# Optimization experiments

Measured on AMD Instinct MI355X. Metric: run time of the kernel, lower is better.

Reference implementation:

```python
import jax, jax.numpy as jnp
import numpy as np

HAD_G = 32  # hadamard_group_size == MX block size (scales are [out, in//32])

# FP4 E2M1 magnitude grid and decision midpoints (round-to-nearest)
_FP4_LEVELS = jnp.array([0.0, 0.5, 1.0, 1.5, 2.0, 3.0, 4.0, 6.0], dtype=jnp.float32)
_FP4_MIDS = jnp.array([0.25, 0.75, 1.25, 1.75, 2.5, 3.5, 5.0], dtype=jnp.float32)


def _hadamard(n: int) -> np.ndarray:
    H = np.array([[1.0]], dtype=np.float32)
    while H.shape[0] < n:
        H = np.block([[H, H], [H, -H]])
    return H * (n ** -0.5)


def mxfp4_quant_dequant(v):
    """MXFP4 quantize-dequantize along the last axis (block of 32).
    v: [..., 32]. Shared power-of-2 scale per block (E8M0, absmax-based),
    elements rounded to nearest FP4 (E2M1) value. Straight-through estimator.
    """
    amax = jnp.max(jnp.abs(v), axis=-1, keepdims=True)
    # scale = 2^(floor(log2(amax)) - emax_fp4), emax_fp4 = 2 (6 = 1.5 * 2^2)
    e = jnp.floor(jnp.log2(jnp.maximum(amax, jnp.float32(1e-30)))) - 2.0
    scale = jnp.exp2(e)
    a = v / scale
    mag = jnp.minimum(jnp.abs(a), 6.0)
    q = _FP4_LEVELS[jnp.digitize(mag, _FP4_MIDS)] * jnp.sign(a)
    deq = q * scale
    # STE: identity gradient through the quantizer (matches custom autograd Fn)
    return v + jax.lax.stop_gradient(deq - v)


def _rotate_quant(t, H):
    """Per-group Hadamard rotation then MXFP4 quant-dequant. t: [N, K]."""
    N, K = t.shape
    tg = t.reshape(N, K // HAD_G, HAD_G)
    tr = jnp.einsum('ngh,hk->ngk', tg, H)  # rotate each 32-group
    return mxfp4_quant_dequant(tr).reshape(N, K)


def setup_inputs() -> dict:
    key = jax.random.key(0)
    kx, kw, kb = jax.random.split(key, 3)
    B, S, K, O = 4, 2048, 4096, 16384
    x = jax.random.normal(kx, (B, S, K), dtype=jnp.float32)
    weight = jax.random.normal(kw, (O, K), dtype=jnp.float32) * 0.02
    bias = jax.random.normal(kb, (O,), dtype=jnp.float32) * 0.01
    fwd_hadamard = jnp.asarray(_hadamard(HAD_G))
    return {"x": x, "weight": weight, "bias": bias, "fwd_hadamard": fwd_hadamard}


def reference(x, weight, bias, fwd_hadamard):
    B, S, K = x.shape
    O = weight.shape[0]
    xq = _rotate_quant(x.reshape(B * S, K), fwd_hadamard)   # deq(q(x H))
    wq = _rotate_quant(weight, fwd_hadamard)                # deq(q(W H))
    # H H^T = I, so (xH)(WH)^T approximates x W^T; GEMM runs on quantized values
    y = xq @ wq.T + bias
    return y.reshape(B, S, O)
```

## Files before the change

### kernel.cpp

```cpp
#include <hip/hip_runtime.h>

typedef unsigned short u16;
typedef unsigned int u32;
typedef unsigned char u8;
typedef int v8i __attribute__((ext_vector_type(8)));
typedef int v4i __attribute__((ext_vector_type(4)));
typedef float v16f __attribute__((ext_vector_type(16)));

#define INV_SQRT32 0.17677669529663688f

#define QOFS_OUT 32768
#define QOFS_SC  36864

__global__ __launch_bounds__(256) void rotquant4_kernel(
    const float* __restrict__ T, u8* __restrict__ Q4, u8* __restrict__ S,
    int K, int ntk, int nkb )
{
    __shared__ __align__(16) u8 smem[37120];

    const int tid  = threadIdx.x;
    const int bid  = blockIdx.x;
    const int rblk = bid / nkb;
    const int kblk = bid - rblk * nkb;
    const int row0 = rblk * 8;
    const int kb0  = kblk * 32;
    const int t0g  = (row0 >> 7) * ntk + (kb0 >> 2);
    const int rl   = row0 & 127;

    {
        const float4* src = (const float4*)T;
#pragma unroll
        for (int j = 0; j < 8; ++j) {
            float4 t = src[(size_t)(row0 + j) * (K >> 2) + (kblk << 8) + tid];
            int kb = tid >> 3, i = tid & 7;
            *(float4*)(smem + j * 4096 + kb * 128 + ((i ^ (kb & 7)) << 4)) = t;
        }
    }
    __syncthreads();

    {
        const int rr = tid >> 5;
        const int kb = tid & 31;

        float v[32];
#pragma unroll
        for (int i = 0; i < 8; ++i) {
            float4 t = *(const float4*)(smem + rr * 4096 + kb * 128
                                        + ((i ^ (kb & 7)) << 4));
            v[i*4+0] = t.x; v[i*4+1] = t.y; v[i*4+2] = t.z; v[i*4+3] = t.w;
        }

#pragma unroll
        for (int s = 1; s < 32; s <<= 1) {
#pragma unroll
            for (int i = 0; i < 32; ++i) {
                if (!(i & s)) {
                    float a = v[i], b = v[i | s];
                    v[i] = a + b;
                    v[i | s] = a - b;
                }
            }
        }

        float amax = 0.f;
#pragma unroll
        for (int i = 0; i < 32; ++i) {
            v[i] *= INV_SQRT32;
            amax = fmaxf(amax, fabsf(v[i]));
        }

        u32 ab = __float_as_uint(amax);
        int be = (int)(ab >> 23);
        u32 w[4] = {0u, 0u, 0u, 0u};
        u8 sbyte = 0;
        if (be >= 3) {
            sbyte = (u8)(be - 2);
            float iscale = __uint_as_float((u32)(256 - be) << 23);
#pragma unroll
            for (int i = 0; i < 32; ++i) {
                float a = v[i] * iscale;
                float m = fminf(fabsf(a), 6.0f);
                int c = (m < 0.25f) ? 0 :
                        (m < 0.75f) ? 1 :
                        (m < 1.25f) ? 2 :
                        (m < 1.75f) ? 3 :
                        (m < 2.5f)  ? 4 :
                        (m < 3.5f)  ? 5 :
                        (m < 5.0f)  ? 6 : 7;
                c |= (int)((__float_as_uint(a) >> 28) & 8u);
                w[i >> 3] |= (u32)c << (4 * (i & 7));
            }
        }

        uint4 p; p.x = w[0]; p.y = w[1]; p.z = w[2]; p.w = w[3];
        *(uint4*)(smem + QOFS_OUT + rr * 512 + (kb >> 2) * 64 + (kb & 3) * 16) = p;
        smem[QOFS_SC + rr * 32 + (kb >> 2) * 4 + (kb & 3)] = sbyte;
    }
    __syncthreads();

    {
        int tileL = tid >> 5, slot = (tid >> 3) & 3, rr = tid & 7;
        uint4 p = *(const uint4*)(smem + QOFS_OUT + rr * 512 + tileL * 64
                                  + slot * 16);
        ((uint4*)Q4)[(size_t)(t0g + tileL) * 512 + slot * 128 + rl + rr] = p;
    }
    if (tid < 64) {
        int tileL = tid >> 3, rr = tid & 7;
        u32 sc = *(const u32*)(smem + QOFS_SC + rr * 32 + tileL * 4);
        ((u32*)S)[(size_t)(t0g + tileL) * 128 + rl + rr] = sc;
    }
}

__device__ __forceinline__ void gload16(const void* g, void* l)
{
    __builtin_amdgcn_global_load_lds(
        (__attribute__((address_space(1))) void*)g,
        (__attribute__((address_space(3))) void*)l, 16, 0, 0);
}
__device__ __forceinline__ void gload4(const void* g, void* l)
{
    __builtin_amdgcn_global_load_lds(
        (__attribute__((address_space(1))) void*)g,
        (__attribute__((address_space(3))) void*)l, 4, 0, 0);
}

#define BUF_BYTES 34816
#define OFS_B     16384
#define OFS_AS    32768
#define OFS_BS    33792

__global__ __launch_bounds__(512, 2) void gemm4_bias(
    const u8* __restrict__ A4, const u8* __restrict__ AS,
    const u8* __restrict__ B4, const u8* __restrict__ BS,
    const float* __restrict__ bias, float* __restrict__ C,
    int M, int N, int K)
{
    __shared__ __align__(16) u8 smem[3 * BUF_BYTES];

    const int tid  = threadIdx.x;
    const int wave = tid >> 6;
    const int lane = tid & 63;
    const int l31  = lane & 31;
    const int lhi  = lane >> 5;
    const int wm   = wave >> 2;
    const int wn   = wave & 3;
    const int ntk  = K >> 7;
    const int NT   = ntk;

    const int nbn = N >> 8;
    const int nbm = M >> 8;
    int bid = blockIdx.x;
    int bm, bn;
    if (((gridDim.x & 7) == 0) && ((nbm & 7) == 0)) {
        int bpc = nbm >> 3;
        int lb  = __builtin_ctz(bpc);
        int c   = bid & 7;
        int r   = bid >> 3;
        bm = c * bpc + (r & (bpc - 1));
        bn = r >> lb;
    } else {
        bn = bid % nbn;
        bm = bid / nbn;
    }

    v16f acc[4][2];
#pragma unroll
    for (int i = 0; i < 4; ++i)
#pragma unroll
        for (int j = 0; j < 2; ++j)
#pragma unroll
            for (int r = 0; r < 16; ++r) acc[i][j][r] = 0.f;

    const size_t aRow0 = (size_t)(2 * bm) * ntk;
    const size_t bRow0 = (size_t)(2 * bn) * ntk;
    const int isA = (wave < 4);
    const int w4  = wave & 3;
    const u8* scB = isA ? AS : BS;
    const size_t scT = (size_t)((isA ? 2 * bm : 2 * bn) + (w4 >> 1)) * ntk;
    const int scInner = (w4 & 1) * 256 + lane * 4;
    const int scDst   = (isA ? OFS_AS : OFS_BS) + w4 * 256;
    const int gOfs = wave * 1024 + lane * 16;
    const int lOfs = wave * 1024;

#define STG_A(bofs, kt, r)                                                    \
    gload16(A4 + ((aRow0 + (size_t)(r) * ntk + (kt)) << 13) + gOfs,           \
            smem + (bofs) + (r) * 8192 + lOfs)
#define STG_B(bofs, kt, r)                                                    \
    gload16(B4 + ((bRow0 + (size_t)(r) * ntk + (kt)) << 13) + gOfs,           \
            smem + (bofs) + OFS_B + (r) * 8192 + lOfs)
#define STG_S(bofs, kt)                                                       \
    gload4(scB + ((scT + (kt)) << 9) + scInner, smem + (bofs) + scDst)
#define STAGE(bofs, kt)                                                       \
    do { STG_A(bofs, kt, 0); STG_A(bofs, kt, 1);                              \
         STG_B(bofs, kt, 0); STG_B(bofs, kt, 1); STG_S(bofs, kt); } while (0)

#define LDSC(dsa, dsb, ofs)                                                   \
    do {                                                                      \
        _Pragma("unroll")                                                     \
        for (int mi = 0; mi < 4; ++mi)                                        \
            dsa[mi] = (*(const u32*)(smem + (ofs) + OFS_AS                    \
                          + (wm * 128 + mi * 32 + l31) * 4)) >> (lhi * 8);    \
        _Pragma("unroll")                                                     \
        for (int ni = 0; ni < 2; ++ni)                                        \
            dsb[ni] = (*(const u32*)(smem + (ofs) + OFS_BS                    \
                          + (wn * 64 + ni * 32 + l31) * 4)) >> (lhi * 8);     \
    } while (0)

#define RD_SET(AF, BF, ks, ofs)                                               \
    do {                                                                      \
        _Pragma("unroll")                                                     \
        for (int mi = 0; mi < 4; ++mi) {                                      \
            v4i t_ = *(const v4i*)(smem + (ofs) + wm * 8192                   \
                                   + ((ks) * 2 + lhi) * 2048                  \
                                   + ((mi) * 32 + l31) * 16);                 \
            AF[mi] = __builtin_shufflevector(t_, t_, 0,1,2,3,-1,-1,-1,-1);    \
        }                                                                     \
        _Pragma("unroll")                                                     \
        for (int ni = 0; ni < 2; ++ni) {                                      \
            v4i t_ = *(const v4i*)(smem + (ofs) + OFS_B + (wn >> 1) * 8192    \
                                   + ((ks) * 2 + lhi) * 2048                  \
                                   + ((wn & 1) * 64 + (ni) * 32 + l31) * 16); \
            BF[ni] = __builtin_shufflevector(t_, t_, 0,1,2,3,-1,-1,-1,-1);    \
        }                                                                     \
    } while (0)

#define MFMA_PH(AF, BF, ks)                                                   \
    do {                                                                      \
        _Pragma("unroll")                                                     \
        for (int mi = 0; mi < 4; ++mi) {                                      \
            int sA_ = (int)((sa[mi] >> ((ks) * 16)) & 0xffu);                 \
            _Pragma("unroll")                                                 \
            for (int ni = 0; ni < 2; ++ni) {                                  \
                int sB_ = (int)((sb[ni] >> ((ks) * 16)) & 0xffu);             \
                acc[mi][ni] = __builtin_amdgcn_mfma_scale_f32_32x32x64_f8f6f4(\
                    AF[mi], BF[ni], acc[mi][ni], 4, 4, 0, sA_, 0, sB_);       \
            }                                                                 \
        }                                                                     \
    } while (0)

    STAGE(0, 0);
    STAGE(BUF_BYTES, 1);
    asm volatile("s_waitcnt vmcnt(5)" ::: "memory");
    __builtin_amdgcn_s_barrier();

    u32 sa[4], sb[2];
    v8i Af[4], Bf[2], Cf[4], Df[2];
    LDSC(sa, sb, 0);
    RD_SET(Af, Bf, 0, 0);

    int cofs = 0, nofs = BUF_BYTES, pofs = 2 * BUF_BYTES;
    for (int t = 0; t < NT; ++t) {
        const bool st = (t + 2 < NT);
        if (st) STAGE(pofs, t + 2);
        RD_SET(Cf, Df, 1, cofs);
        __builtin_amdgcn_s_setprio(1);
        MFMA_PH(Af, Bf, 0);
        __builtin_amdgcn_s_setprio(0);
        if (st) asm volatile("s_waitcnt vmcnt(5)" ::: "memory");
        else    asm volatile("s_waitcnt vmcnt(0)" ::: "memory");
        __builtin_amdgcn_s_barrier();
        u32 tsa[4] = {0,0,0,0}, tsb[2] = {0,0};
        if (t + 1 < NT) {
            LDSC(tsa, tsb, nofs);
            RD_SET(Af, Bf, 0, nofs);
        }
        __builtin_amdgcn_s_setprio(1);
        MFMA_PH(Cf, Df, 1);
        __builtin_amdgcn_s_setprio(0);
#pragma unroll
        for (int i = 0; i < 4; ++i) sa[i] = tsa[i];
#pragma unroll
        for (int i = 0; i < 2; ++i) sb[i] = tsb[i];
        int old = cofs;
        cofs = nofs; nofs = pofs; pofs = old;
    }

    const int cb = bn * 256 + wn * 64;
    const int rb = bm * 256 + wm * 128;
#pragma unroll
    for (int ni = 0; ni < 2; ++ni) {
        float bb = bias[cb + ni * 32 + l31];
#pragma unroll
        for (int mi = 0; mi < 4; ++mi) {
#pragma unroll
            for (int reg = 0; reg < 16; ++reg) {
                int row = (reg & 3) + 8 * (reg >> 2) + 4 * lhi;
                C[(size_t)(rb + mi * 32 + row) * N + cb + ni * 32 + l31]
                    = acc[mi][ni][reg] + bb;
            }
        }
    }
#undef STG_A
#undef STG_B
#undef STG_S
#undef STAGE
#undef LDSC
#undef RD_SET
#undef MFMA_PH
}

extern "C" void kernel_launch(void* const* d_in, const int* in_sizes, int n_in,
                              void* d_out, int out_size, void* d_ws, size_t ws_size,
                              hipStream_t stream)
{
    const float* x    = (const float*)d_in[0];
    const float* w    = (const float*)d_in[1];
    const float* bias = (const float*)d_in[2];

    const int O = in_sizes[2];
    const int K = in_sizes[1] / O;
    const int M = in_sizes[0] / K;

    u8* x4 = (u8*)d_ws;
    u8* w4 = x4 + (size_t)M * (K / 2);
    u8* xs = w4 + (size_t)O * (K / 2);
    u8* ws = xs + (size_t)M * (K / 32);

    const int ntk = K / 128;
    const int nkb = K / 1024;
    rotquant4_kernel<<<(M / 8) * nkb, 256, 0, stream>>>(x, x4, xs, K, ntk, nkb);
    rotquant4_kernel<<<(O / 8) * nkb, 256, 0, stream>>>(w, w4, ws, K, ntk, nkb);

    dim3 grid((M / 256) * (O / 256));
    gemm4_bias<<<grid, 512, 0, stream>>>(x4, xs, w4, ws, bias, (float*)d_out,
                                         M, O, K);
}
```

Before: 490.9 us.

## Unroll GEMM main loop by three with constant LDS buffer offsets

The scaled-MFMA FP4 GEMM main loop is unrolled by three, so each triple-buffer slot's LDS offset is a compile-time constant. Per-thread LDS base addresses for fragments and scales are computed once before the loop. Each tile now reads both k-halves' fragments and scales up front, then issues all 16 MFMAs, with one wait and barrier per tile. The old scheme prefetched the next tile's first half into registers across the barrier; that is dropped, which cuts address arithmetic and register rotation but relies on the compiler to overlap LDS reads with MFMAs. The tail handling assumes the tile count leaves remainder two when divided by three.

Result: faster. 454.7 us (-7.4%).

```diff
diff --git a/kernel.cpp b/kernel.cpp
--- a/kernel.cpp
+++ b/kernel.cpp
@@ -128,6 +128,9 @@
 #define OFS_B     16384
 #define OFS_AS    32768
 #define OFS_BS    33792
+#define BB0 0
+#define BB1 BUF_BYTES
+#define BB2 (2 * BUF_BYTES)
 
 __global__ __launch_bounds__(512, 2) void gemm4_bias(
     const u8* __restrict__ A4, const u8* __restrict__ AS,
@@ -182,6 +185,13 @@
     const int gOfs = wave * 1024 + lane * 16;
     const int lOfs = wave * 1024;
 
+    const int aRB   = wm * 8192 + lhi * 2048 + l31 * 16;
+    const int bRB   = OFS_B + (wn >> 1) * 8192 + lhi * 2048
+                      + (wn & 1) * 1024 + l31 * 16;
+    const int asB   = OFS_AS + wm * 512 + l31 * 4;
+    const int bsB   = OFS_BS + wn * 256 + l31 * 4;
+    const int shamt = lhi * 8;
+
 #define STG_A(bofs, kt, r)                                                    \
     gload16(A4 + ((aRow0 + (size_t)(r) * ntk + (kt)) << 13) + gOfs,           \
             smem + (bofs) + (r) * 8192 + lOfs)
@@ -194,86 +204,68 @@
     do { STG_A(bofs, kt, 0); STG_A(bofs, kt, 1);                              \
          STG_B(bofs, kt, 0); STG_B(bofs, kt, 1); STG_S(bofs, kt); } while (0)
 
-#define LDSC(dsa, dsb, ofs)                                                   \
+#define MK8(x) __builtin_shufflevector(x, x, 0, 1, 2, 3, -1, -1, -1, -1)
+#define MFMA1(mi, ni, AF, BF, SA, SB)                                         \
+    acc[mi][ni] = __builtin_amdgcn_mfma_scale_f32_32x32x64_f8f6f4(            \
+        MK8(AF), MK8(BF), acc[mi][ni], 4, 4, 0, (int)(SA), 0, (int)(SB))
+#define CL8(A0, A1, A2, A3, Bx0, Bx1, S0, S1, S2, S3, T0, T1)                 \
     do {                                                                      \
-        _Pragma("unroll")                                                     \
-        for (int mi = 0; mi < 4; ++mi)                                        \
-            dsa[mi] = (*(const u32*)(smem + (ofs) + OFS_AS                    \
-                          + (wm * 128 + mi * 32 + l31) * 4)) >> (lhi * 8);    \
-        _Pragma("unroll")                                                     \
-        for (int ni = 0; ni < 2; ++ni)                                        \
-            dsb[ni] = (*(const u32*)(smem + (ofs) + OFS_BS                    \
-                          + (wn * 64 + ni * 32 + l31) * 4)) >> (lhi * 8);     \
+        MFMA1(0, 0, A0, Bx0, S0, T0); MFMA1(0, 1, A0, Bx1, S0, T1);           \
+        MFMA1(1, 0, A1, Bx0, S1, T0); MFMA1(1, 1, A1, Bx1, S1, T1);           \
+        MFMA1(2, 0, A2, Bx0, S2, T0); MFMA1(2, 1, A2, Bx1, S2, T1);           \
+        MFMA1(3, 0, A3, Bx0, S3, T0); MFMA1(3, 1, A3, Bx1, S3, T1);           \
     } while (0)
 
-#define RD_SET(AF, BF, ks, ofs)                                               \
+#define TILE(CO, PO, kt, ST, FINAL)                                           \
     do {                                                                      \
-        _Pragma("unroll")                                                     \
-        for (int mi = 0; mi < 4; ++mi) {                                      \
-            v4i t_ = *(const v4i*)(smem + (ofs) + wm * 8192                   \
-                                   + ((ks) * 2 + lhi) * 2048                  \
-                                   + ((mi) * 32 + l31) * 16);                 \
-            AF[mi] = __builtin_shufflevector(t_, t_, 0,1,2,3,-1,-1,-1,-1);    \
-        }                                                                     \
-        _Pragma("unroll")                                                     \
-        for (int ni = 0; ni < 2; ++ni) {                                      \
-            v4i t_ = *(const v4i*)(smem + (ofs) + OFS_B + (wn >> 1) * 8192    \
-                                   + ((ks) * 2 + lhi) * 2048                  \
-                                   + ((wn & 1) * 64 + (ni) * 32 + l31) * 16); \
-            BF[ni] = __builtin_shufflevector(t_, t_, 0,1,2,3,-1,-1,-1,-1);    \
+        if (ST) STAGE(PO, (kt) + 2);                                          \
+        u32 sa0 = (*(const u32*)(smem + (CO) + asB      )) >> shamt;          \
+        u32 sa1 = (*(const u32*)(smem + (CO) + asB + 128)) >> shamt;          \
+        u32 sa2 = (*(const u32*)(smem + (CO) + asB + 256)) >> shamt;          \
+        u32 sa3 = (*(const u32*)(smem + (CO) + asB + 384)) >> shamt;          \
+        u32 sb0 = (*(const u32*)(smem + (CO) + bsB      )) >> shamt;          \
+        u32 sb1 = (*(const u32*)(smem + (CO) + bsB + 128)) >> shamt;          \
+        v4i a00 = *(const v4i*)(smem + (CO) + aRB       );                    \
+        v4i a01 = *(const v4i*)(smem + (CO) + aRB +  512);                    \
+        v4i a02 = *(const v4i*)(smem + (CO) + aRB + 1024);                    \
+        v4i a03 = *(const v4i*)(smem + (CO) + aRB + 1536);                    \
+        v4i b00 = *(const v4i*)(smem + (CO) + bRB       );                    \
+        v4i b01 = *(const v4i*)(smem + (CO) + bRB +  512);                    \
+        v4i a10 = *(const v4i*)(smem + (CO) + aRB + 4096);                    \
+        v4i a11 = *(const v4i*)(smem + (CO) + aRB + 4608);                    \
+        v4i a12 = *(const v4i*)(smem + (CO) + aRB + 5120);                    \
+        v4i a13 = *(const v4i*)(smem + (CO) + aRB + 5632);                    \
+        v4i b10 = *(const v4i*)(smem + (CO) + bRB + 4096);                    \
+        v4i b11 = *(const v4i*)(smem + (CO) + bRB + 4608);                    \
+        __builtin_amdgcn_s_setprio(1);                                        \
+        CL8(a00, a01, a02, a03, b00, b01,                                     \
+            sa0 & 0xffu, sa1 & 0xffu, sa2 & 0xffu, sa3 & 0xffu,               \
+            sb0 & 0xffu, sb1 & 0xffu);                                        \
+        CL8(a10, a11, a12, a13, b10, b11,                                     \
+            (sa0 >> 16) & 0xffu, (sa1 >> 16) & 0xffu,                         \
+            (sa2 >> 16) & 0xffu, (sa3 >> 16) & 0xffu,                         \
+            (sb0 >> 16) & 0xffu, (sb1 >> 16) & 0xffu);                        \
+        __builtin_amdgcn_s_setprio(0);                                        \
+        if (!(FINAL)) {                                                       \
+            if (ST) { asm volatile("s_waitcnt vmcnt(5)" ::: "memory"); }      \
+            else    { asm volatile("s_waitcnt vmcnt(0)" ::: "memory"); }      \
+            __builtin_amdgcn_s_barrier();                                     \
         }                                                                     \
     } while (0)
 
-#define MFMA_PH(AF, BF, ks)                                                   \
-    do {                                                                      \
-        _Pragma("unroll")                                                     \
-        for (int mi = 0; mi < 4; ++mi) {                                      \
-            int sA_ = (int)((sa[mi] >> ((ks) * 16)) & 0xffu);                 \
-            _Pragma("unroll")                                                 \
-            for (int ni = 0; ni < 2; ++ni) {                                  \
-                int sB_ = (int)((sb[ni] >> ((ks) * 16)) & 0xffu);             \
-                acc[mi][ni] = __builtin_amdgcn_mfma_scale_f32_32x32x64_f8f6f4(\
-                    AF[mi], BF[ni], acc[mi][ni], 4, 4, 0, sA_, 0, sB_);       \
-            }                                                                 \
-        }                                                                     \
-    } while (0)
-
-    STAGE(0, 0);
-    STAGE(BUF_BYTES, 1);
+    STAGE(BB0, 0);
+    STAGE(BB1, 1);
     asm volatile("s_waitcnt vmcnt(5)" ::: "memory");
     __builtin_amdgcn_s_barrier();
 
-    u32 sa[4], sb[2];
-    v8i Af[4], Bf[2], Cf[4], Df[2];
-    LDSC(sa, sb, 0);
-    RD_SET(Af, Bf, 0, 0);
-
-    int cofs = 0, nofs = BUF_BYTES, pofs = 2 * BUF_BYTES;
-    for (int t = 0; t < NT; ++t) {
-        const bool st = (t + 2 < NT);
-        if (st) STAGE(pofs, t + 2);
-        RD_SET(Cf, Df, 1, cofs);
-        __builtin_amdgcn_s_setprio(1);
-        MFMA_PH(Af, Bf, 0);
-        __builtin_amdgcn_s_setprio(0);
-        if (st) asm volatile("s_waitcnt vmcnt(5)" ::: "memory");
-        else    asm volatile("s_waitcnt vmcnt(0)" ::: "memory");
-        __builtin_amdgcn_s_barrier();
-        u32 tsa[4] = {0,0,0,0}, tsb[2] = {0,0};
-        if (t + 1 < NT) {
-            LDSC(tsa, tsb, nofs);
-            RD_SET(Af, Bf, 0, nofs);
-        }
-        __builtin_amdgcn_s_setprio(1);
-        MFMA_PH(Cf, Df, 1);
-        __builtin_amdgcn_s_setprio(0);
-#pragma unroll
-        for (int i = 0; i < 4; ++i) sa[i] = tsa[i];
-#pragma unroll
-        for (int i = 0; i < 2; ++i) sb[i] = tsb[i];
-        int old = cofs;
-        cofs = nofs; nofs = pofs; pofs = old;
-    }
+#pragma unroll 1
+    for (int t = 0; t + 2 < NT; t += 3) {
+        TILE(BB0, BB2, t + 0, true, false);
+        TILE(BB1, BB0, t + 1, true, false);
+        TILE(BB2, BB1, t + 2, true, false);
+    }
+    TILE(BB0, BB2, NT - 2, false, false);
+    TILE(BB1, BB2, NT - 1, false, true);
 
     const int cb = bn * 256 + wn * 64;
     const int rb = bm * 256 + wm * 128;
@@ -294,9 +286,10 @@
 #undef STG_B
 #undef STG_S
 #undef STAGE
-#undef LDSC
-#undef RD_SET
-#undef MFMA_PH
+#undef MK8
+#undef MFMA1
+#undef CL8
+#undef TILE
 }
 
 extern "C" void kernel_launch(void* const* d_in, const int* in_sizes, int n_in,
```
